# Kernel tuning notes

Measured on AMD Instinct MI355X. Metric: run time of the kernel, lower is better.

The kernel has to match this reference:

```python
import jax, jax.numpy as jnp
import numpy as np

B, C, H, W = 4, 192, 128, 128
K = 4                       # cross-scan directions (all identical tokens since L=1, but distinct weights)
DSTATE = 8
DTRANK = max(8, C // 16)    # 12
EPS = 1e-5


def _ln(x, w, b):
    mu = jnp.mean(x, axis=-1, keepdims=True)
    var = jnp.var(x, axis=-1, keepdims=True)
    return (x - mu) * jax.lax.rsqrt(var + EPS) * w + b


def setup_inputs() -> dict:
    key = jax.random.key(0)
    ks = jax.random.split(key, 16)
    s_in = 1.0 / np.sqrt(C)
    inp = {
        "x": jax.random.normal(ks[0], (B, C, H, W), jnp.float32),
        "norm_w": 1.0 + 0.02 * jax.random.normal(ks[1], (C,), jnp.float32),
        "norm_b": 0.02 * jax.random.normal(ks[2], (C,), jnp.float32),
        "w_in": s_in * jax.random.normal(ks[3], (2 * C, C), jnp.float32),
        "ssm_in_w": s_in * jax.random.normal(ks[4], (2 * C, C), jnp.float32),
        "x_proj_w": s_in * jax.random.normal(ks[5], (K, DTRANK + 2 * DSTATE, C), jnp.float32),
        "dt_w": (1.0 / np.sqrt(DTRANK)) * jax.random.normal(ks[6], (K, C, DTRANK), jnp.float32),
        "dt_b": 0.1 * jax.random.normal(ks[7], (K, C), jnp.float32),
        "A_logs": jnp.log(jnp.broadcast_to(jnp.arange(1, DSTATE + 1, dtype=jnp.float32), (K * C, DSTATE))),
        "Ds": jnp.ones((K * C,), jnp.float32),
        "out_norm_w": 1.0 + 0.02 * jax.random.normal(ks[8], (C,), jnp.float32),
        "out_norm_b": 0.02 * jax.random.normal(ks[9], (C,), jnp.float32),
        "ssm_out_w": s_in * jax.random.normal(ks[10], (C, C), jnp.float32),
        "w_out": s_in * jax.random.normal(ks[11], (C, C), jnp.float32),
    }
    return inp


def reference(x, norm_w, norm_b, w_in, ssm_in_w, x_proj_w, dt_w, dt_b,
              A_logs, Ds, out_norm_w, out_norm_b, ssm_out_w, w_out):
    # (B,C,H,W) -> (B,H,W,C)
    xh = jnp.transpose(x, (0, 2, 3, 1))
    xn = _ln(xh, norm_w, norm_b)
    p = xn @ w_in.T                         # (B,H,W,2C)
    x1, x2 = p[..., :C], p[..., C:]

    # ---- SS2D (v2, d_conv=1) on per-pixel sequences of length 1 ----
    u = x1 @ ssm_in_w.T                     # (B,H,W,2C)
    xss, z = u[..., :C], u[..., C:]
    z = jax.nn.silu(z)
    xss = jax.nn.silu(xss)

    # x_proj per direction: (B,H,W,K,dt_rank+2*d_state)
    xd = jnp.einsum('bhwd,kcd->bhwkc', xss, x_proj_w)
    dtr = xd[..., :DTRANK]
    Bv = xd[..., DTRANK:DTRANK + DSTATE]
    Cv = xd[..., DTRANK + DSTATE:]
    dt = jax.nn.softplus(jnp.einsum('bhwkr,kdr->bhwkd', dtr, dt_w) + dt_b)

    # Selective scan with L=1 and h0=0: h = dt*B*xss; y_k = sum_s C_s*h_s + D*xss
    # => y = xss * sum_k ( (B . C)_k * dt_k + D_k ).  A = -exp(A_logs) never enters (L=1).
    bc = jnp.sum(Bv * Cv, axis=-1)          # (B,H,W,K)
    gain = jnp.sum(bc[..., None] * dt + Ds.reshape(K, C), axis=-2)  # (B,H,W,C)
    y = xss * gain
    y = _ln(y, out_norm_w, out_norm_b)
    y = y * z
    s = y @ ssm_out_w.T                     # SS2D out_proj

    # ---- block gating + out_proj + residual ----
    o = (s * jax.nn.silu(x2)) @ w_out.T
    return x + jnp.transpose(o, (0, 3, 1, 2))
```

## Files before the change

### kernel.cpp

```cpp
#include <hip/hip_runtime.h>
#include <hip/hip_bf16.h>
#include <math.h>


#define CC    192
#define HH    128
#define WW    128
#define NK    4
#define DST   8
#define DTR   12
#define TP    32
#define SP    200
#define NTH   256

typedef __attribute__((ext_vector_type(8))) short bh8;
typedef __attribute__((ext_vector_type(4))) float f4;

#define OFF_WIN    0
#define OFF_SSMIN  73728
#define OFF_XPROJ  147456
#define OFF_SSMOUT 168960
#define OFF_WOUT   205824
#define OFF_DTW    242688
#define WTOT2      267264

#define MFMA(va, vb, vc) __builtin_amdgcn_mfma_f32_16x16x32_bf16(va, vb, vc, 0, 0, 0)

__device__ __forceinline__ float bf2f(unsigned short u) {
    union { unsigned int i; float f; } v; v.i = ((unsigned int)u) << 16; return v.f;
}
__device__ __forceinline__ unsigned short f2bf(float f) {
    __hip_bfloat16 h = __float2bfloat16(f);
    unsigned short u; __builtin_memcpy(&u, &h, 2); return u;
}
__device__ __forceinline__ unsigned int pk2(float a, float b) {
    return (unsigned int)f2bf(a) | ((unsigned int)f2bf(b) << 16);
}
__device__ __forceinline__ float lo16(unsigned int u) { return bf2f((unsigned short)(u & 0xffffu)); }
__device__ __forceinline__ float hi16(unsigned int u) { return bf2f((unsigned short)(u >> 16)); }

#define LOG2E 1.44269504f
#define LN2   0.69314718f
__device__ __forceinline__ float silu_fast(float x) {
    float e = __builtin_amdgcn_exp2f(-LOG2E * x);
    return x * __builtin_amdgcn_rcpf(1.f + e);
}
__device__ __forceinline__ float softplus_fast(float x) {
    float e = __builtin_amdgcn_exp2f(-LOG2E * fabsf(x));
    return fmaxf(x, 0.f) + LN2 * __builtin_amdgcn_logf(1.f + e);
}

extern "C" __global__ void prep_w(const float* __restrict__ w_in,
                                  const float* __restrict__ ssm_in_w,
                                  const float* __restrict__ x_proj_w,
                                  const float* __restrict__ ssm_out_w,
                                  const float* __restrict__ w_out,
                                  const float* __restrict__ dt_w,
                                  const float* __restrict__ dt_b,
                                  const float* __restrict__ Ds,
                                  unsigned short* __restrict__ wb)
{
    int i = blockIdx.x * NTH + threadIdx.x;
    if (i < OFF_DTW) {
        float v;
        if      (i < OFF_XPROJ ) v = (i < OFF_SSMIN) ? w_in[i] : ssm_in_w[i - OFF_SSMIN];
        else if (i < OFF_SSMOUT) v = x_proj_w[i - OFF_XPROJ];
        else if (i < OFF_WOUT  ) v = ssm_out_w[i - OFF_SSMOUT];
        else                     v = w_out[i - OFF_WOUT];
        wb[i] = f2bf(v);
    } else if (i < WTOT2) {
        int j  = i - OFF_DTW;
        int r  = j & 31;
        int kc = j >> 5;
        float v = (r < DTR) ? dt_w[kc * DTR + r]
                            : (r == 31 ? dt_b[kc] : 0.f);
        wb[i] = f2bf(v);
    } else if (i < WTOT2 + CC) {
        int c = i - WTOT2;
        float* dsum = (float*)(wb + WTOT2);
        dsum[c] = Ds[c] + Ds[CC + c] + Ds[2*CC + c] + Ds[3*CC + c];
    }
}

extern "C" __global__ void __launch_bounds__(NTH, 4)
mamba_fused(const float* __restrict__ x,
            const float* __restrict__ norm_w,  const float* __restrict__ norm_b,
            const float* __restrict__ out_norm_w, const float* __restrict__ out_norm_b,
            const unsigned short* __restrict__ wsb,
            float* __restrict__ out)
{
    __shared__ __align__(16) unsigned short sA [TP][SP];
    __shared__ __align__(16) unsigned short sB [TP][SP];
    __shared__ __align__(16) unsigned short sZ [TP][CC];
    __shared__ float sred [TP][8];
    __shared__ float sred2[TP][8];
    __shared__ float smu[TP];
    __shared__ float srs[TP];
    __shared__ __align__(16) float sbcT[NK][TP];

    const int tid  = threadIdx.x;
    const int lane = tid & 63;
    const int wave = tid >> 6;
    const int frow = lane & 15;
    const int kb   = lane >> 4;
    const int pxb  = kb * 4;

    const int t   = blockIdx.x;
    const int b   = t >> 9;
    const int rem = t & 511;
    const int h   = rem >> 2;
    const int w0g = (rem & 3) * TP;

    const float* dsum = (const float*)(wsb + WTOT2);

    uint2 x2a0, x2a1, x2a2, x2b0, x2b1, x2b2;

    {
        const int px = tid & 31, part = tid >> 5;
        float sum = 0.f, sq = 0.f;
        const size_t base = (((size_t)b * CC) * HH + h) * WW + w0g + px;
        for (int i = 0; i < 24; ++i) {
            int c = part * 24 + i;
            float v = x[base + (size_t)c * (HH * WW)];
            sum += v; sq += v * v;
            sA[px][c] = f2bf(v);
        }
        sred[px][part] = sum; sred2[px][part] = sq;
        __syncthreads();
        if (part == 0) {
            float s = 0.f, q = 0.f;
            for (int j = 0; j < 8; ++j) { s += sred[px][j]; q += sred2[px][j]; }
            float mu  = s * (1.f / CC);
            float var = q * (1.f / CC) - mu * mu;
            smu[px] = mu; srs[px] = rsqrtf(var + 1e-5f);
        }
        __syncthreads();
        const float mu = smu[px], rs = srs[px];
        for (int i = 0; i < 24; ++i) {
            int c = part * 24 + i;
            float v = bf2f(sA[px][c]);
            v = (v - mu) * rs * norm_w[c] + norm_b[c];
            sA[px][c] = f2bf(v);
        }
        __syncthreads();
    }

    auto load_a = [&](const unsigned short* sSrc, bh8 a[2][6]) {
#pragma unroll
        for (int m = 0; m < 2; ++m)
#pragma unroll
            for (int ks = 0; ks < 6; ++ks)
                a[m][ks] = *(const bh8*)(sSrc + (m * 16 + frow) * SP + ks * 32 + kb * 8);
    };
    auto gemm_pair = [&](const bh8 a[2][6], const unsigned short* wB, int n0, int n1,
                         f4& p0, f4& p1, f4& q0, f4& q1) {
        const unsigned short* wp0 = wB + (size_t)(n0 + frow) * CC + kb * 8;
        const unsigned short* wp1 = wB + (size_t)(n1 + frow) * CC + kb * 8;
#pragma unroll
        for (int ks = 0; ks < 6; ++ks) {
            bh8 b0 = *(const bh8*)(wp0 + ks * 32);
            bh8 b1 = *(const bh8*)(wp1 + ks * 32);
            p0 = MFMA(a[0][ks], b0, p0);
            p1 = MFMA(a[1][ks], b0, p1);
            q0 = MFMA(a[0][ks], b1, q0);
            q1 = MFMA(a[1][ks], b1, q1);
        }
    };
    auto gemm_one = [&](const bh8 a[2][6], const unsigned short* wB, int n0,
                        f4& p0, f4& p1) {
        const unsigned short* wp = wB + (size_t)(n0 + frow) * CC + kb * 8;
#pragma unroll
        for (int ks = 0; ks < 6; ++ks) {
            bh8 bf = *(const bh8*)(wp + ks * 32);
            p0 = MFMA(a[0][ks], bf, p0);
            p1 = MFMA(a[1][ks], bf, p1);
        }
    };
    auto st_sB = [&](int o, const f4& c0, const f4& c1) {
#pragma unroll
        for (int r = 0; r < 4; ++r) {
            sB[pxb + r][o]      = f2bf(c0[r]);
            sB[16 + pxb + r][o] = f2bf(c1[r]);
        }
    };
    auto st_sA_silu = [&](int o, const f4& c0, const f4& c1) {
#pragma unroll
        for (int r = 0; r < 4; ++r) {
            sA[pxb + r][o]      = f2bf(silu_fast(c0[r]));
            sA[16 + pxb + r][o] = f2bf(silu_fast(c1[r]));
        }
    };
    auto st_sZ_silu = [&](int oc, const f4& c0, const f4& c1) {
#pragma unroll
        for (int r = 0; r < 4; ++r) {
            sZ[pxb + r][oc]      = f2bf(silu_fast(c0[r]));
            sZ[16 + pxb + r][oc] = f2bf(silu_fast(c1[r]));
        }
    };
    auto pack_silu = [&](const f4& c) {
        return make_uint2(pk2(silu_fast(c[0]), silu_fast(c[1])),
                          pk2(silu_fast(c[2]), silu_fast(c[3])));
    };

    {
        bh8 a[2][6]; load_a(&sA[0][0], a);
        const unsigned short* wB = wsb + OFF_WIN;
        {
            f4 p0={0,0,0,0},p1={0,0,0,0},q0={0,0,0,0},q1={0,0,0,0};
            gemm_pair(a, wB, wave * 16, (wave + 4) * 16, p0, p1, q0, q1);
            st_sB(wave * 16 + frow, p0, p1);
            st_sB((wave + 4) * 16 + frow, q0, q1);
        }
        {
            f4 p0={0,0,0,0},p1={0,0,0,0},q0={0,0,0,0},q1={0,0,0,0};
            gemm_pair(a, wB, (wave + 8) * 16, (wave + 12) * 16, p0, p1, q0, q1);
            st_sB((wave + 8) * 16 + frow, p0, p1);
            x2a0 = pack_silu(q0); x2b0 = pack_silu(q1);
        }
        {
            f4 p0={0,0,0,0},p1={0,0,0,0},q0={0,0,0,0},q1={0,0,0,0};
            gemm_pair(a, wB, (wave + 16) * 16, (wave + 20) * 16, p0, p1, q0, q1);
            x2a1 = pack_silu(p0); x2b1 = pack_silu(p1);
            x2a2 = pack_silu(q0); x2b2 = pack_silu(q1);
        }
    }
    __syncthreads();

    {
        bh8 a[2][6]; load_a(&sB[0][0], a);
        const unsigned short* wB = wsb + OFF_SSMIN;
        {
            f4 p0={0,0,0,0},p1={0,0,0,0},q0={0,0,0,0},q1={0,0,0,0};
            gemm_pair(a, wB, wave * 16, (wave + 4) * 16, p0, p1, q0, q1);
            st_sA_silu(wave * 16 + frow, p0, p1);
            st_sA_silu((wave + 4) * 16 + frow, q0, q1);
        }
        {
            f4 p0={0,0,0,0},p1={0,0,0,0},q0={0,0,0,0},q1={0,0,0,0};
            gemm_pair(a, wB, (wave + 8) * 16, (wave + 12) * 16, p0, p1, q0, q1);
            st_sA_silu((wave + 8) * 16 + frow, p0, p1);
            st_sZ_silu((wave + 12) * 16 + frow - CC, q0, q1);
        }
        {
            f4 p0={0,0,0,0},p1={0,0,0,0},q0={0,0,0,0},q1={0,0,0,0};
            gemm_pair(a, wB, (wave + 16) * 16, (wave + 20) * 16, p0, p1, q0, q1);
            st_sZ_silu((wave + 16) * 16 + frow - CC, p0, p1);
            st_sZ_silu((wave + 20) * 16 + frow - CC, q0, q1);
        }
    }
    __syncthreads();

    {
        bh8 a[2][6]; load_a(&sA[0][0], a);
        const unsigned short* wB = wsb + OFF_XPROJ;
        f4 p0={0,0,0,0},p1={0,0,0,0},q0={0,0,0,0},q1={0,0,0,0};
        gemm_pair(a, wB, wave * 16, (wave + 4) * 16, p0, p1, q0, q1);
        st_sB(wave * 16 + frow, p0, p1);
        st_sB((wave + 4) * 16 + frow, q0, q1);
    }
    __syncthreads();

    if (tid < TP * NK) {
        int px = tid & 31, k = tid >> 5;
        float a = 0.f;
        for (int s = 0; s < DST; ++s)
            a += bf2f(sB[px][k*28 + DTR + s]) * bf2f(sB[px][k*28 + DTR + DST + s]);
        sbcT[k][px] = a;
    }
    __syncthreads();

    {
        bh8 adt[NK][2];
#pragma unroll
        for (int k = 0; k < NK; ++k)
#pragma unroll
            for (int m = 0; m < 2; ++m) {
                const unsigned short* rp = &sB[m * 16 + frow][k * 28];
                bh8 v;
                if (kb == 0) {
                    ushort4 lo = *(const ushort4*)(rp);
                    ushort4 hi = *(const ushort4*)(rp + 4);
                    v = bh8{(short)lo.x,(short)lo.y,(short)lo.z,(short)lo.w,
                            (short)hi.x,(short)hi.y,(short)hi.z,(short)hi.w};
                } else if (kb == 1) {
                    ushort4 lo = *(const ushort4*)(rp + 8);
                    v = bh8{(short)lo.x,(short)lo.y,(short)lo.z,(short)lo.w,0,0,0,0};
                } else if (kb == 2) {
                    v = bh8{0,0,0,0,0,0,0,0};
                } else {
                    v = bh8{0,0,0,0,0,0,0,(short)0x3F80};
                }
                adt[k][m] = v;
            }
        const unsigned short* wDT = wsb + OFF_DTW;
        for (int ct = wave; ct < 12; ct += 4) {
            int c = ct * 16 + frow;
            f4 g0 = {0.f,0.f,0.f,0.f}, g1 = {0.f,0.f,0.f,0.f};
#pragma unroll
            for (int k = 0; k < NK; ++k) {
                bh8 bf = *(const bh8*)(wDT + (((size_t)(k * CC + c)) << 5) + kb * 8);
                f4 d0 = {0.f,0.f,0.f,0.f}, d1 = {0.f,0.f,0.f,0.f};
                d0 = MFMA(adt[k][0], bf, d0);
                d1 = MFMA(adt[k][1], bf, d1);
                f4 bc0 = *(const f4*)(&sbcT[k][pxb]);
                f4 bc1 = *(const f4*)(&sbcT[k][16 + pxb]);
#pragma unroll
                for (int r = 0; r < 4; ++r) {
                    g0[r] += bc0[r] * softplus_fast(d0[r]);
                    g1[r] += bc1[r] * softplus_fast(d1[r]);
                }
            }
            float ds = dsum[c];
#pragma unroll
            for (int r = 0; r < 4; ++r) {
                float y0 = bf2f(sA[pxb + r][c]) * (g0[r] + ds);
                sA[pxb + r][c] = f2bf(y0);
                float y1 = bf2f(sA[16 + pxb + r][c]) * (g1[r] + ds);
                sA[16 + pxb + r][c] = f2bf(y1);
            }
        }
    }
    __syncthreads();

    {
        const int px = tid & 31, part = tid >> 5;
        float sum = 0.f, sq = 0.f;
        for (int i = 0; i < 24; ++i) {
            int c = part * 24 + i;
            float v = bf2f(sA[px][c]);
            sum += v; sq += v * v;
        }
        sred[px][part] = sum; sred2[px][part] = sq;
        __syncthreads();
        if (part == 0) {
            float s = 0.f, q = 0.f;
            for (int j = 0; j < 8; ++j) { s += sred[px][j]; q += sred2[px][j]; }
            float mu  = s * (1.f / CC);
            float var = q * (1.f / CC) - mu * mu;
            smu[px] = mu; srs[px] = rsqrtf(var + 1e-5f);
        }
        __syncthreads();
        const float mu = smu[px], rs = srs[px];
        for (int i = 0; i < 24; ++i) {
            int c = part * 24 + i;
            float v = bf2f(sA[px][c]);
            v = (v - mu) * rs * out_norm_w[c] + out_norm_b[c];
            v *= bf2f(sZ[px][c]);
            sA[px][c] = f2bf(v);
        }
        __syncthreads();
    }

    {
        bh8 a[2][6]; load_a(&sA[0][0], a);
        const unsigned short* wB = wsb + OFF_SSMOUT;
        {
            f4 p0={0,0,0,0},p1={0,0,0,0},q0={0,0,0,0},q1={0,0,0,0};
            gemm_pair(a, wB, wave * 16, (wave + 4) * 16, p0, p1, q0, q1);
            int o0 = wave * 16 + frow, o1 = (wave + 4) * 16 + frow;
            sB[pxb + 0][o0]      = f2bf(p0[0] * lo16(x2a0.x));
            sB[pxb + 1][o0]      = f2bf(p0[1] * hi16(x2a0.x));
            sB[pxb + 2][o0]      = f2bf(p0[2] * lo16(x2a0.y));
            sB[pxb + 3][o0]      = f2bf(p0[3] * hi16(x2a0.y));
            sB[16 + pxb + 0][o0] = f2bf(p1[0] * lo16(x2b0.x));
            sB[16 + pxb + 1][o0] = f2bf(p1[1] * hi16(x2b0.x));
            sB[16 + pxb + 2][o0] = f2bf(p1[2] * lo16(x2b0.y));
            sB[16 + pxb + 3][o0] = f2bf(p1[3] * hi16(x2b0.y));
            sB[pxb + 0][o1]      = f2bf(q0[0] * lo16(x2a1.x));
            sB[pxb + 1][o1]      = f2bf(q0[1] * hi16(x2a1.x));
            sB[pxb + 2][o1]      = f2bf(q0[2] * lo16(x2a1.y));
            sB[pxb + 3][o1]      = f2bf(q0[3] * hi16(x2a1.y));
            sB[16 + pxb + 0][o1] = f2bf(q1[0] * lo16(x2b1.x));
            sB[16 + pxb + 1][o1] = f2bf(q1[1] * hi16(x2b1.x));
            sB[16 + pxb + 2][o1] = f2bf(q1[2] * lo16(x2b1.y));
            sB[16 + pxb + 3][o1] = f2bf(q1[3] * hi16(x2b1.y));
        }
        {
            f4 p0={0,0,0,0},p1={0,0,0,0};
            gemm_one(a, wB, (wave + 8) * 16, p0, p1);
            int o = (wave + 8) * 16 + frow;
            sB[pxb + 0][o]      = f2bf(p0[0] * lo16(x2a2.x));
            sB[pxb + 1][o]      = f2bf(p0[1] * hi16(x2a2.x));
            sB[pxb + 2][o]      = f2bf(p0[2] * lo16(x2a2.y));
            sB[pxb + 3][o]      = f2bf(p0[3] * hi16(x2a2.y));
            sB[16 + pxb + 0][o] = f2bf(p1[0] * lo16(x2b2.x));
            sB[16 + pxb + 1][o] = f2bf(p1[1] * hi16(x2b2.x));
            sB[16 + pxb + 2][o] = f2bf(p1[2] * lo16(x2b2.y));
            sB[16 + pxb + 3][o] = f2bf(p1[3] * hi16(x2b2.y));
        }
    }
    __syncthreads();

    {
        bh8 a[2][6]; load_a(&sB[0][0], a);
        const unsigned short* wB = wsb + OFF_WOUT;
        auto st_out = [&](int o, const f4& c0, const f4& c1) {
            const size_t g0 = (((size_t)b * CC + o) * HH + h) * WW + w0g;
#pragma unroll
            for (int r = 0; r < 4; ++r) {
                out[g0 + pxb + r]      = x[g0 + pxb + r]      + c0[r];
                out[g0 + 16 + pxb + r] = x[g0 + 16 + pxb + r] + c1[r];
            }
        };
        {
            f4 p0={0,0,0,0},p1={0,0,0,0},q0={0,0,0,0},q1={0,0,0,0};
            gemm_pair(a, wB, wave * 16, (wave + 4) * 16, p0, p1, q0, q1);
            st_out(wave * 16 + frow, p0, p1);
            st_out((wave + 4) * 16 + frow, q0, q1);
        }
        {
            f4 p0={0,0,0,0},p1={0,0,0,0};
            gemm_one(a, wB, (wave + 8) * 16, p0, p1);
            st_out((wave + 8) * 16 + frow, p0, p1);
        }
    }
}

extern "C" void kernel_launch(void* const* d_in, const int* in_sizes, int n_in,
                              void* d_out, int out_size, void* d_ws, size_t ws_size,
                              hipStream_t stream) {
    const float* x          = (const float*)d_in[0];
    const float* norm_w     = (const float*)d_in[1];
    const float* norm_b     = (const float*)d_in[2];
    const float* w_in       = (const float*)d_in[3];
    const float* ssm_in_w   = (const float*)d_in[4];
    const float* x_proj_w   = (const float*)d_in[5];
    const float* dt_w       = (const float*)d_in[6];
    const float* dt_b       = (const float*)d_in[7];
    const float* Ds         = (const float*)d_in[9];
    const float* out_norm_w = (const float*)d_in[10];
    const float* out_norm_b = (const float*)d_in[11];
    const float* ssm_out_w  = (const float*)d_in[12];
    const float* w_out      = (const float*)d_in[13];

    unsigned short* wb = (unsigned short*)d_ws;
    int prep_n = WTOT2 + CC;
    prep_w<<<dim3((prep_n + NTH - 1) / NTH), dim3(NTH), 0, stream>>>(
        w_in, ssm_in_w, x_proj_w, ssm_out_w, w_out, dt_w, dt_b, Ds, wb);

    mamba_fused<<<dim3(2048), dim3(NTH), 0, stream>>>(
        x, norm_w, norm_b, out_norm_w, out_norm_b, wb, (float*)d_out);
}
```

Baseline: 152.6 us.

## Shrink LDS footprint by reusing one activation buffer and keeping z in registers

Replaces the three shared tiles (sA, sB, sZ) with a single in-place activation buffer sX plus a small sXD buffer for the x_proj outputs. The silu(z) values are held in packed registers instead of shared memory, and extra barriers are added so the buffer can be safely overwritten after its A-fragments are loaded. The output LayerNorm now uses per-lane accumulation and wave shuffles instead of a shared-memory reduction. The intent is to cut LDS per block to raise occupancy, but launch bounds drop from 4 to 3 and register pressure grows, which may offset that gain.

```diff
diff --git a/kernel.cpp b/kernel.cpp
--- a/kernel.cpp
+++ b/kernel.cpp
@@ -10,8 +10,9 @@
 #define DST   8
 #define DTR   12
 #define TP    32
+#define NTH   256
 #define SP    200
-#define NTH   256
+#define SD    112
 
 typedef __attribute__((ext_vector_type(8))) short bh8;
 typedef __attribute__((ext_vector_type(4))) float f4;
@@ -40,14 +41,14 @@
 __device__ __forceinline__ float hi16(unsigned int u) { return bf2f((unsigned short)(u >> 16)); }
 
 #define LOG2E 1.44269504f
-#define LN2   0.69314718f
+#define LN2C  0.69314718f
 __device__ __forceinline__ float silu_fast(float x) {
     float e = __builtin_amdgcn_exp2f(-LOG2E * x);
     return x * __builtin_amdgcn_rcpf(1.f + e);
 }
 __device__ __forceinline__ float softplus_fast(float x) {
     float e = __builtin_amdgcn_exp2f(-LOG2E * fabsf(x));
-    return fmaxf(x, 0.f) + LN2 * __builtin_amdgcn_logf(1.f + e);
+    return fmaxf(x, 0.f) + LN2C * __builtin_amdgcn_logf(1.f + e);
 }
 
 extern "C" __global__ void prep_w(const float* __restrict__ w_in,
@@ -82,16 +83,15 @@
     }
 }
 
-extern "C" __global__ void __launch_bounds__(NTH, 4)
+extern "C" __global__ void __launch_bounds__(NTH, 3)
 mamba_fused(const float* __restrict__ x,
             const float* __restrict__ norm_w,  const float* __restrict__ norm_b,
             const float* __restrict__ out_norm_w, const float* __restrict__ out_norm_b,
             const unsigned short* __restrict__ wsb,
             float* __restrict__ out)
 {
-    __shared__ __align__(16) unsigned short sA [TP][SP];
-    __shared__ __align__(16) unsigned short sB [TP][SP];
-    __shared__ __align__(16) unsigned short sZ [TP][CC];
+    __shared__ __align__(16) unsigned short sX [TP][SP];
+    __shared__ __align__(16) unsigned short sXD[TP][SD];
     __shared__ float sred [TP][8];
     __shared__ float sred2[TP][8];
     __shared__ float smu[TP];
@@ -113,7 +113,8 @@
 
     const float* dsum = (const float*)(wsb + WTOT2);
 
-    uint2 x2a0, x2a1, x2a2, x2b0, x2b1, x2b2;
+    unsigned int x2p0[3][2], x2p1[3][2];
+    unsigned int zp0 [3][2], zp1 [3][2];
 
     {
         const int px = tid & 31, part = tid >> 5;
@@ -123,7 +124,7 @@
             int c = part * 24 + i;
             float v = x[base + (size_t)c * (HH * WW)];
             sum += v; sq += v * v;
-            sA[px][c] = f2bf(v);
+            sX[px][c] = f2bf(v);
         }
         sred[px][part] = sum; sred2[px][part] = sq;
         __syncthreads();
@@ -138,21 +139,22 @@
         const float mu = smu[px], rs = srs[px];
         for (int i = 0; i < 24; ++i) {
             int c = part * 24 + i;
-            float v = bf2f(sA[px][c]);
+            float v = bf2f(sX[px][c]);
             v = (v - mu) * rs * norm_w[c] + norm_b[c];
-            sA[px][c] = f2bf(v);
-        }
-        __syncthreads();
-    }
-
-    auto load_a = [&](const unsigned short* sSrc, bh8 a[2][6]) {
+            sX[px][c] = f2bf(v);
+        }
+        __syncthreads();
+    }
+
+    bh8 a[2][6];
+    auto load_a = [&]() {
 #pragma unroll
         for (int m = 0; m < 2; ++m)
 #pragma unroll
             for (int ks = 0; ks < 6; ++ks)
-                a[m][ks] = *(const bh8*)(sSrc + (m * 16 + frow) * SP + ks * 32 + kb * 8);
+                a[m][ks] = *(const bh8*)(&sX[m * 16 + frow][ks * 32 + kb * 8]);
     };
-    auto gemm_pair = [&](const bh8 a[2][6], const unsigned short* wB, int n0, int n1,
+    auto gemm_pair = [&](const unsigned short* wB, int n0, int n1,
                          f4& p0, f4& p1, f4& q0, f4& q1) {
         const unsigned short* wp0 = wB + (size_t)(n0 + frow) * CC + kb * 8;
         const unsigned short* wp1 = wB + (size_t)(n1 + frow) * CC + kb * 8;
@@ -166,8 +168,7 @@
             q1 = MFMA(a[1][ks], b1, q1);
         }
     };
-    auto gemm_one = [&](const bh8 a[2][6], const unsigned short* wB, int n0,
-                        f4& p0, f4& p1) {
+    auto gemm_one = [&](const unsigned short* wB, int n0, f4& p0, f4& p1) {
         const unsigned short* wp = wB + (size_t)(n0 + frow) * CC + kb * 8;
 #pragma unroll
         for (int ks = 0; ks < 6; ++ks) {
@@ -176,96 +177,119 @@
             p1 = MFMA(a[1][ks], bf, p1);
         }
     };
-    auto st_sB = [&](int o, const f4& c0, const f4& c1) {
+    auto st_sX = [&](int o, const f4& c0, const f4& c1) {
 #pragma unroll
         for (int r = 0; r < 4; ++r) {
-            sB[pxb + r][o]      = f2bf(c0[r]);
-            sB[16 + pxb + r][o] = f2bf(c1[r]);
+            sX[pxb + r][o]      = f2bf(c0[r]);
+            sX[16 + pxb + r][o] = f2bf(c1[r]);
         }
     };
-    auto st_sA_silu = [&](int o, const f4& c0, const f4& c1) {
+    auto st_sX_silu = [&](int o, const f4& c0, const f4& c1) {
 #pragma unroll
         for (int r = 0; r < 4; ++r) {
-            sA[pxb + r][o]      = f2bf(silu_fast(c0[r]));
-            sA[16 + pxb + r][o] = f2bf(silu_fast(c1[r]));
+            sX[pxb + r][o]      = f2bf(silu_fast(c0[r]));
+            sX[16 + pxb + r][o] = f2bf(silu_fast(c1[r]));
         }
     };
-    auto st_sZ_silu = [&](int oc, const f4& c0, const f4& c1) {
-#pragma unroll
-        for (int r = 0; r < 4; ++r) {
-            sZ[pxb + r][oc]      = f2bf(silu_fast(c0[r]));
-            sZ[16 + pxb + r][oc] = f2bf(silu_fast(c1[r]));
-        }
-    };
-    auto pack_silu = [&](const f4& c) {
-        return make_uint2(pk2(silu_fast(c[0]), silu_fast(c[1])),
-                          pk2(silu_fast(c[2]), silu_fast(c[3])));
-    };
-
-    {
-        bh8 a[2][6]; load_a(&sA[0][0], a);
+
+    {
+        load_a();
+        __syncthreads();
         const unsigned short* wB = wsb + OFF_WIN;
         {
             f4 p0={0,0,0,0},p1={0,0,0,0},q0={0,0,0,0},q1={0,0,0,0};
-            gemm_pair(a, wB, wave * 16, (wave + 4) * 16, p0, p1, q0, q1);
-            st_sB(wave * 16 + frow, p0, p1);
-            st_sB((wave + 4) * 16 + frow, q0, q1);
-        }
-        {
-            f4 p0={0,0,0,0},p1={0,0,0,0},q0={0,0,0,0},q1={0,0,0,0};
-            gemm_pair(a, wB, (wave + 8) * 16, (wave + 12) * 16, p0, p1, q0, q1);
-            st_sB((wave + 8) * 16 + frow, p0, p1);
-            x2a0 = pack_silu(q0); x2b0 = pack_silu(q1);
-        }
-        {
-            f4 p0={0,0,0,0},p1={0,0,0,0},q0={0,0,0,0},q1={0,0,0,0};
-            gemm_pair(a, wB, (wave + 16) * 16, (wave + 20) * 16, p0, p1, q0, q1);
-            x2a1 = pack_silu(p0); x2b1 = pack_silu(p1);
-            x2a2 = pack_silu(q0); x2b2 = pack_silu(q1);
-        }
-    }
-    __syncthreads();
-
-    {
-        bh8 a[2][6]; load_a(&sB[0][0], a);
+            gemm_pair(wB, wave * 16, (wave + 4) * 16, p0, p1, q0, q1);
+            st_sX(wave * 16 + frow, p0, p1);
+            st_sX((wave + 4) * 16 + frow, q0, q1);
+        }
+        {
+            f4 p0={0,0,0,0},p1={0,0,0,0},q0={0,0,0,0},q1={0,0,0,0};
+            gemm_pair(wB, (wave + 8) * 16, (wave + 12) * 16, p0, p1, q0, q1);
+            st_sX((wave + 8) * 16 + frow, p0, p1);
+            x2p0[0][0] = pk2(silu_fast(q0[0]), silu_fast(q0[1]));
+            x2p0[0][1] = pk2(silu_fast(q0[2]), silu_fast(q0[3]));
+            x2p1[0][0] = pk2(silu_fast(q1[0]), silu_fast(q1[1]));
+            x2p1[0][1] = pk2(silu_fast(q1[2]), silu_fast(q1[3]));
+        }
+        {
+            f4 p0={0,0,0,0},p1={0,0,0,0},q0={0,0,0,0},q1={0,0,0,0};
+            gemm_pair(wB, (wave + 16) * 16, (wave + 20) * 16, p0, p1, q0, q1);
+            x2p0[1][0] = pk2(silu_fast(p0[0]), silu_fast(p0[1]));
+            x2p0[1][1] = pk2(silu_fast(p0[2]), silu_fast(p0[3]));
+            x2p1[1][0] = pk2(silu_fast(p1[0]), silu_fast(p1[1]));
+            x2p1[1][1] = pk2(silu_fast(p1[2]), silu_fast(p1[3]));
+            x2p0[2][0] = pk2(silu_fast(q0[0]), silu_fast(q0[1]));
+            x2p0[2][1] = pk2(silu_fast(q0[2]), silu_fast(q0[3]));
+            x2p1[2][0] = pk2(silu_fast(q1[0]), silu_fast(q1[1]));
+            x2p1[2][1] = pk2(silu_fast(q1[2]), silu_fast(q1[3]));
+        }
+        __syncthreads();
+    }
+
+    {
+        load_a();
+        __syncthreads();
         const unsigned short* wB = wsb + OFF_SSMIN;
         {
             f4 p0={0,0,0,0},p1={0,0,0,0},q0={0,0,0,0},q1={0,0,0,0};
-            gemm_pair(a, wB, wave * 16, (wave + 4) * 16, p0, p1, q0, q1);
-            st_sA_silu(wave * 16 + frow, p0, p1);
-            st_sA_silu((wave + 4) * 16 + frow, q0, q1);
-        }
-        {
-            f4 p0={0,0,0,0},p1={0,0,0,0},q0={0,0,0,0},q1={0,0,0,0};
-            gemm_pair(a, wB, (wave + 8) * 16, (wave + 12) * 16, p0, p1, q0, q1);
-            st_sA_silu((wave + 8) * 16 + frow, p0, p1);
-            st_sZ_silu((wave + 12) * 16 + frow - CC, q0, q1);
-        }
-        {
-            f4 p0={0,0,0,0},p1={0,0,0,0},q0={0,0,0,0},q1={0,0,0,0};
-            gemm_pair(a, wB, (wave + 16) * 16, (wave + 20) * 16, p0, p1, q0, q1);
-            st_sZ_silu((wave + 16) * 16 + frow - CC, p0, p1);
-            st_sZ_silu((wave + 20) * 16 + frow - CC, q0, q1);
-        }
-    }
-    __syncthreads();
-
-    {
-        bh8 a[2][6]; load_a(&sA[0][0], a);
+            gemm_pair(wB, wave * 16, (wave + 4) * 16, p0, p1, q0, q1);
+            st_sX_silu(wave * 16 + frow, p0, p1);
+            st_sX_silu((wave + 4) * 16 + frow, q0, q1);
+        }
+        {
+            f4 p0={0,0,0,0},p1={0,0,0,0},q0={0,0,0,0},q1={0,0,0,0};
+            gemm_pair(wB, (wave + 8) * 16, (wave + 12) * 16, p0, p1, q0, q1);
+            st_sX_silu((wave + 8) * 16 + frow, p0, p1);
+            zp0[0][0] = pk2(silu_fast(q0[0]), silu_fast(q0[1]));
+            zp0[0][1] = pk2(silu_fast(q0[2]), silu_fast(q0[3]));
+            zp1[0][0] = pk2(silu_fast(q1[0]), silu_fast(q1[1]));
+            zp1[0][1] = pk2(silu_fast(q1[2]), silu_fast(q1[3]));
+        }
+        {
+            f4 p0={0,0,0,0},p1={0,0,0,0},q0={0,0,0,0},q1={0,0,0,0};
+            gemm_pair(wB, (wave + 16) * 16, (wave + 20) * 16, p0, p1, q0, q1);
+            zp0[1][0] = pk2(silu_fast(p0[0]), silu_fast(p0[1]));
+            zp0[1][1] = pk2(silu_fast(p0[2]), silu_fast(p0[3]));
+            zp1[1][0] = pk2(silu_fast(p1[0]), silu_fast(p1[1]));
+            zp1[1][1] = pk2(silu_fast(p1[2]), silu_fast(p1[3]));
+            zp0[2][0] = pk2(silu_fast(q0[0]), silu_fast(q0[1]));
+            zp0[2][1] = pk2(silu_fast(q0[2]), silu_fast(q0[3]));
+            zp1[2][0] = pk2(silu_fast(q1[0]), silu_fast(q1[1]));
+            zp1[2][1] = pk2(silu_fast(q1[2]), silu_fast(q1[3]));
+        }
+        __syncthreads();
+    }
+
+    {
+        load_a();
         const unsigned short* wB = wsb + OFF_XPROJ;
         f4 p0={0,0,0,0},p1={0,0,0,0},q0={0,0,0,0},q1={0,0,0,0};
-        gemm_pair(a, wB, wave * 16, (wave + 4) * 16, p0, p1, q0, q1);
-        st_sB(wave * 16 + frow, p0, p1);
-        st_sB((wave + 4) * 16 + frow, q0, q1);
-    }
-    __syncthreads();
+        gemm_pair(wB, wave * 16, (wave + 4) * 16, p0, p1, q0, q1);
+        {
+            int o = wave * 16 + frow;
+#pragma unroll
+            for (int r = 0; r < 4; ++r) {
+                sXD[pxb + r][o]      = f2bf(p0[r]);
+                sXD[16 + pxb + r][o] = f2bf(p1[r]);
+            }
+        }
+        if (wave < 3) {
+            int o = (wave + 4) * 16 + frow;
+#pragma unroll
+            for (int r = 0; r < 4; ++r) {
+                sXD[pxb + r][o]      = f2bf(q0[r]);
+                sXD[16 + pxb + r][o] = f2bf(q1[r]);
+            }
+        }
+        __syncthreads();
+    }
 
     if (tid < TP * NK) {
         int px = tid & 31, k = tid >> 5;
-        float a = 0.f;
+        float acc = 0.f;
         for (int s = 0; s < DST; ++s)
-            a += bf2f(sB[px][k*28 + DTR + s]) * bf2f(sB[px][k*28 + DTR + DST + s]);
-        sbcT[k][px] = a;
+            acc += bf2f(sXD[px][k*28 + DTR + s]) * bf2f(sXD[px][k*28 + DTR + DST + s]);
+        sbcT[k][px] = acc;
     }
     __syncthreads();
 
@@ -275,26 +299,28 @@
         for (int k = 0; k < NK; ++k)
 #pragma unroll
             for (int m = 0; m < 2; ++m) {
-                const unsigned short* rp = &sB[m * 16 + frow][k * 28];
-                bh8 v;
+                const unsigned short* rp = &sXD[m * 16 + frow][k * 28];
+                bh8 vv;
                 if (kb == 0) {
                     ushort4 lo = *(const ushort4*)(rp);
                     ushort4 hi = *(const ushort4*)(rp + 4);
-                    v = bh8{(short)lo.x,(short)lo.y,(short)lo.z,(short)lo.w,
-                            (short)hi.x,(short)hi.y,(short)hi.z,(short)hi.w};
+                    vv = bh8{(short)lo.x,(short)lo.y,(short)lo.z,(short)lo.w,
+                             (short)hi.x,(short)hi.y,(short)hi.z,(short)hi.w};
                 } else if (kb == 1) {
                     ushort4 lo = *(const ushort4*)(rp + 8);
-                    v = bh8{(short)lo.x,(short)lo.y,(short)lo.z,(short)lo.w,0,0,0,0};
+                    vv = bh8{(short)lo.x,(short)lo.y,(short)lo.z,(short)lo.w,0,0,0,0};
                 } else if (kb == 2) {
-                    v = bh8{0,0,0,0,0,0,0,0};
+                    vv = bh8{0,0,0,0,0,0,0,0};
                 } else {
-                    v = bh8{0,0,0,0,0,0,0,(short)0x3F80};
+                    vv = bh8{0,0,0,0,0,0,0,(short)0x3F80};
                 }
-                adt[k][m] = v;
+                adt[k][m] = vv;
             }
         const unsigned short* wDT = wsb + OFF_DTW;
-        for (int ct = wave; ct < 12; ct += 4) {
-            int c = ct * 16 + frow;
+#pragma unroll
+        for (int j = 0; j < 3; ++j) {
+            int ct = wave + 4 * j;
+            int c  = ct * 16 + frow;
             f4 g0 = {0.f,0.f,0.f,0.f}, g1 = {0.f,0.f,0.f,0.f};
 #pragma unroll
             for (int k = 0; k < NK; ++k) {
@@ -313,86 +339,113 @@
             float ds = dsum[c];
 #pragma unroll
             for (int r = 0; r < 4; ++r) {
-                float y0 = bf2f(sA[pxb + r][c]) * (g0[r] + ds);
-                sA[pxb + r][c] = f2bf(y0);
-                float y1 = bf2f(sA[16 + pxb + r][c]) * (g1[r] + ds);
-                sA[16 + pxb + r][c] = f2bf(y1);
+                float y0 = bf2f(sX[pxb + r][c]) * (g0[r] + ds);
+                sX[pxb + r][c] = f2bf(y0);
+                float y1 = bf2f(sX[16 + pxb + r][c]) * (g1[r] + ds);
+                sX[16 + pxb + r][c] = f2bf(y1);
             }
         }
     }
     __syncthreads();
 
-    {
-        const int px = tid & 31, part = tid >> 5;
-        float sum = 0.f, sq = 0.f;
-        for (int i = 0; i < 24; ++i) {
-            int c = part * 24 + i;
-            float v = bf2f(sA[px][c]);
-            sum += v; sq += v * v;
-        }
-        sred[px][part] = sum; sred2[px][part] = sq;
-        __syncthreads();
-        if (part == 0) {
-            float s = 0.f, q = 0.f;
-            for (int j = 0; j < 8; ++j) { s += sred[px][j]; q += sred2[px][j]; }
-            float mu  = s * (1.f / CC);
-            float var = q * (1.f / CC) - mu * mu;
-            smu[px] = mu; srs[px] = rsqrtf(var + 1e-5f);
-        }
-        __syncthreads();
-        const float mu = smu[px], rs = srs[px];
-        for (int i = 0; i < 24; ++i) {
-            int c = part * 24 + i;
-            float v = bf2f(sA[px][c]);
-            v = (v - mu) * rs * out_norm_w[c] + out_norm_b[c];
-            v *= bf2f(sZ[px][c]);
-            sA[px][c] = f2bf(v);
-        }
-        __syncthreads();
-    }
-
-    {
-        bh8 a[2][6]; load_a(&sA[0][0], a);
+    f4 mu0, rs0, mu1, rs1;
+    {
+        f4 s0 = {0,0,0,0}, q0v = {0,0,0,0}, s1 = {0,0,0,0}, q1v = {0,0,0,0};
+#pragma unroll
+        for (int ct2 = 0; ct2 < 12; ++ct2) {
+            int c = ct2 * 16 + frow;
+#pragma unroll
+            for (int r = 0; r < 4; ++r) {
+                float ya = bf2f(sX[pxb + r][c]);
+                float yb = bf2f(sX[16 + pxb + r][c]);
+                s0[r] += ya; q0v[r] += ya * ya;
+                s1[r] += yb; q1v[r] += yb * yb;
+            }
+        }
+#pragma unroll
+        for (int m = 1; m < 16; m <<= 1) {
+#pragma unroll
+            for (int r = 0; r < 4; ++r) {
+                s0[r]  += __shfl_xor(s0[r],  m);
+                q0v[r] += __shfl_xor(q0v[r], m);
+                s1[r]  += __shfl_xor(s1[r],  m);
+                q1v[r] += __shfl_xor(q1v[r], m);
+            }
+        }
+#pragma unroll
+        for (int r = 0; r < 4; ++r) {
+            mu0[r] = s0[r] * (1.f / CC);
+            rs0[r] = rsqrtf(q0v[r] * (1.f / CC) - mu0[r] * mu0[r] + 1e-5f);
+            mu1[r] = s1[r] * (1.f / CC);
+            rs1[r] = rsqrtf(q1v[r] * (1.f / CC) - mu1[r] * mu1[r] + 1e-5f);
+        }
+    }
+    __syncthreads();
+
+    {
+#pragma unroll
+        for (int j = 0; j < 3; ++j) {
+            int ct = wave + 4 * j;
+            int c  = ct * 16 + frow;
+            float wn = out_norm_w[c], bn = out_norm_b[c];
+#pragma unroll
+            for (int r = 0; r < 4; ++r) {
+                float za = (r < 2) ? ((r & 1) ? hi16(zp0[j][0]) : lo16(zp0[j][0]))
+                                   : ((r & 1) ? hi16(zp0[j][1]) : lo16(zp0[j][1]));
+                float zb = (r < 2) ? ((r & 1) ? hi16(zp1[j][0]) : lo16(zp1[j][0]))
+                                   : ((r & 1) ? hi16(zp1[j][1]) : lo16(zp1[j][1]));
+                float ya = bf2f(sX[pxb + r][c]);
+                float yb = bf2f(sX[16 + pxb + r][c]);
+                sX[pxb + r][c]      = f2bf(((ya - mu0[r]) * rs0[r] * wn + bn) * za);
+                sX[16 + pxb + r][c] = f2bf(((yb - mu1[r]) * rs1[r] * wn + bn) * zb);
+            }
+        }
+    }
+    __syncthreads();
+
+    {
+        load_a();
+        __syncthreads();
         const unsigned short* wB = wsb + OFF_SSMOUT;
         {
             f4 p0={0,0,0,0},p1={0,0,0,0},q0={0,0,0,0},q1={0,0,0,0};
-            gemm_pair(a, wB, wave * 16, (wave + 4) * 16, p0, p1, q0, q1);
+            gemm_pair(wB, wave * 16, (wave + 4) * 16, p0, p1, q0, q1);
             int o0 = wave * 16 + frow, o1 = (wave + 4) * 16 + frow;
-            sB[pxb + 0][o0]      = f2bf(p0[0] * lo16(x2a0.x));
-            sB[pxb + 1][o0]      = f2bf(p0[1] * hi16(x2a0.x));
-            sB[pxb + 2][o0]      = f2bf(p0[2] * lo16(x2a0.y));
-            sB[pxb + 3][o0]      = f2bf(p0[3] * hi16(x2a0.y));
-            sB[16 + pxb + 0][o0] = f2bf(p1[0] * lo16(x2b0.x));
-            sB[16 + pxb + 1][o0] = f2bf(p1[1] * hi16(x2b0.x));
-            sB[16 + pxb + 2][o0] = f2bf(p1[2] * lo16(x2b0.y));
-            sB[16 + pxb + 3][o0] = f2bf(p1[3] * hi16(x2b0.y));
-            sB[pxb + 0][o1]      = f2bf(q0[0] * lo16(x2a1.x));
-            sB[pxb + 1][o1]      = f2bf(q0[1] * hi16(x2a1.x));
-            sB[pxb + 2][o1]      = f2bf(q0[2] * lo16(x2a1.y));
-            sB[pxb + 3][o1]      = f2bf(q0[3] * hi16(x2a1.y));
-            sB[16 + pxb + 0][o1] = f2bf(q1[0] * lo16(x2b1.x));
-            sB[16 + pxb + 1][o1] = f2bf(q1[1] * hi16(x2b1.x));
-            sB[16 + pxb + 2][o1] = f2bf(q1[2] * lo16(x2b1.y));
-            sB[16 + pxb + 3][o1] = f2bf(q1[3] * hi16(x2b1.y));
+            sX[pxb + 0][o0]      = f2bf(p0[0] * lo16(x2p0[0][0]));
+            sX[pxb + 1][o0]      = f2bf(p0[1] * hi16(x2p0[0][0]));
+            sX[pxb + 2][o0]      = f2bf(p0[2] * lo16(x2p0[0][1]));
+            sX[pxb + 3][o0]      = f2bf(p0[3] * hi16(x2p0[0][1]));
+            sX[16 + pxb + 0][o0] = f2bf(p1[0] * lo16(x2p1[0][0]));
+            sX[16 + pxb + 1][o0] = f2bf(p1[1] * hi16(x2p1[0][0]));
+            sX[16 + pxb + 2][o0] = f2bf(p1[2] * lo16(x2p1[0][1]));
+            sX[16 + pxb + 3][o0] = f2bf(p1[3] * hi16(x2p1[0][1]));
+            sX[pxb + 0][o1]      = f2bf(q0[0] * lo16(x2p0[1][0]));
+            sX[pxb + 1][o1]      = f2bf(q0[1] * hi16(x2p0[1][0]));
+            sX[pxb + 2][o1]      = f2bf(q0[2] * lo16(x2p0[1][1]));
+            sX[pxb + 3][o1]      = f2bf(q0[3] * hi16(x2p0[1][1]));
+            sX[16 + pxb + 0][o1] = f2bf(q1[0] * lo16(x2p1[1][0]));
+            sX[16 + pxb + 1][o1] = f2bf(q1[1] * hi16(x2p1[1][0]));
+            sX[16 + pxb + 2][o1] = f2bf(q1[2] * lo16(x2p1[1][1]));
+            sX[16 + pxb + 3][o1] = f2bf(q1[3] * hi16(x2p1[1][1]));
         }
         {
             f4 p0={0,0,0,0},p1={0,0,0,0};
-            gemm_one(a, wB, (wave + 8) * 16, p0, p1);
+            gemm_one(wB, (wave + 8) * 16, p0, p1);
             int o = (wave + 8) * 16 + frow;
-            sB[pxb + 0][o]      = f2bf(p0[0] * lo16(x2a2.x));
-            sB[pxb + 1][o]      = f2bf(p0[1] * hi16(x2a2.x));
-            sB[pxb + 2][o]      = f2bf(p0[2] * lo16(x2a2.y));
-            sB[pxb + 3][o]      = f2bf(p0[3] * hi16(x2a2.y));
-            sB[16 + pxb + 0][o] = f2bf(p1[0] * lo16(x2b2.x));
-            sB[16 + pxb + 1][o] = f2bf(p1[1] * hi16(x2b2.x));
-            sB[16 + pxb + 2][o] = f2bf(p1[2] * lo16(x2b2.y));
-            sB[16 + pxb + 3][o] = f2bf(p1[3] * hi16(x2b2.y));
-        }
-    }
-    __syncthreads();
-
-    {
-        bh8 a[2][6]; load_a(&sB[0][0], a);
+            sX[pxb + 0][o]      = f2bf(p0[0] * lo16(x2p0[2][0]));
+            sX[pxb + 1][o]      = f2bf(p0[1] * hi16(x2p0[2][0]));
+            sX[pxb + 2][o]      = f2bf(p0[2] * lo16(x2p0[2][1]));
+            sX[pxb + 3][o]      = f2bf(p0[3] * hi16(x2p0[2][1]));
+            sX[16 + pxb + 0][o] = f2bf(p1[0] * lo16(x2p1[2][0]));
+            sX[16 + pxb + 1][o] = f2bf(p1[1] * hi16(x2p1[2][0]));
+            sX[16 + pxb + 2][o] = f2bf(p1[2] * lo16(x2p1[2][1]));
+            sX[16 + pxb + 3][o] = f2bf(p1[3] * hi16(x2p1[2][1]));
+        }
+        __syncthreads();
+    }
+
+    {
+        load_a();
         const unsigned short* wB = wsb + OFF_WOUT;
         auto st_out = [&](int o, const f4& c0, const f4& c1) {
             const size_t g0 = (((size_t)b * CC + o) * HH + h) * WW + w0g;
@@ -404,13 +457,13 @@
         };
         {
             f4 p0={0,0,0,0},p1={0,0,0,0},q0={0,0,0,0},q1={0,0,0,0};
-            gemm_pair(a, wB, wave * 16, (wave + 4) * 16, p0, p1, q0, q1);
+            gemm_pair(wB, wave * 16, (wave + 4) * 16, p0, p1, q0, q1);
             st_out(wave * 16 + frow, p0, p1);
             st_out((wave + 4) * 16 + frow, q0, q1);
         }
         {
             f4 p0={0,0,0,0},p1={0,0,0,0};
-            gemm_one(a, wB, (wave + 8) * 16, p0, p1);
+            gemm_one(wB, (wave + 8) * 16, p0, p1);
             st_out((wave + 8) * 16 + frow, p0, p1);
         }
     }
```

Result: slower. 171.6 us (+12.4%).
